# Kernel optimization log

Measured on AMD Instinct MI355X. Metric: run time of the kernel, lower is better.

The kernel has to match this reference:

```python
import jax, jax.numpy as jnp
import numpy as np

DIM = 128
NUM_HEADS = 4
WH, WW = 7, 7
N = WH * WW
B_ = 4096


def _relative_position_index():
    coords_h = np.arange(WH)
    coords_w = np.arange(WW)
    coords = np.stack(np.meshgrid(coords_h, coords_w, indexing='ij'))  # (2, Wh, Ww)
    coords_flat = coords.reshape(2, -1)  # (2, N)
    rel = coords_flat[:, :, None] - coords_flat[:, None, :]  # (2, N, N)
    rel = rel.transpose(1, 2, 0).astype(np.int32)  # (N, N, 2)
    rel[:, :, 0] += WH - 1
    rel[:, :, 1] += WW - 1
    rel[:, :, 0] *= 2 * WW - 1
    return rel.sum(-1)  # (N, N) int32


def setup_inputs() -> dict:
    key = jax.random.key(0)
    ks = jax.random.split(key, 6)
    x = jax.random.normal(ks[0], (B_, N, DIM), dtype=jnp.float32)
    # torch nn.Linear-style params: weight (out, in), bias (out,)
    qkv_w = jax.random.normal(ks[1], (3 * DIM, DIM), dtype=jnp.float32) * (DIM ** -0.5)
    qkv_b = jnp.zeros((3 * DIM,), dtype=jnp.float32)
    proj_w = jax.random.normal(ks[2], (DIM, DIM), dtype=jnp.float32) * (DIM ** -0.5)
    proj_b = jnp.zeros((DIM,), dtype=jnp.float32)
    rpb_table = jax.random.normal(ks[3], ((2 * WH - 1) * (2 * WW - 1), NUM_HEADS), dtype=jnp.float32) * 0.02
    rpi = jnp.asarray(_relative_position_index())  # (N, N) int32
    return {"x": x, "qkv_w": qkv_w, "qkv_b": qkv_b, "proj_w": proj_w,
            "proj_b": proj_b, "rpb_table": rpb_table, "rpi": rpi}


def reference(x, qkv_w, qkv_b, proj_w, proj_b, rpb_table, rpi):
    b, n, c = x.shape
    h = NUM_HEADS
    hd = c // h
    scale = hd ** -0.5
    qkv = jnp.einsum('bnc,oc->bno', x, qkv_w) + qkv_b  # (B_, N, 3C)
    qkv = qkv.reshape(b, n, 3, h, hd)
    q = jnp.transpose(qkv[:, :, 0], (0, 2, 1, 3))  # (b, h, n, hd)
    k = jnp.transpose(qkv[:, :, 1], (0, 2, 1, 3))
    v = jnp.transpose(qkv[:, :, 2], (0, 2, 1, 3))
    attn = jnp.einsum('bhnd,bhmd->bhnm', q * scale, k)  # (b, h, n, n)
    bias = rpb_table[rpi.reshape(-1)].reshape(n, n, h)  # gather bias per pair
    attn = attn + jnp.transpose(bias, (2, 0, 1))[None]  # (1, h, n, n)
    attn = jax.nn.softmax(attn, axis=-1)
    out = jnp.einsum('bhnm,bhmd->bhnd', attn, v)
    out = jnp.transpose(out, (0, 2, 1, 3)).reshape(b, n, c)
    out = jnp.einsum('bnc,oc->bno', out, proj_w) + proj_b
    return out
```

## Files before the change

### kernel.cpp

```cpp
#include <hip/hip_runtime.h>
#include <hip/hip_bf16.h>

typedef __attribute__((ext_vector_type(8))) short s16x8;
typedef __attribute__((ext_vector_type(4))) float f32x4;
typedef unsigned short u16;

#define NTOK 49
#define CDIM 128
#define NH 4
#define NWIN 4096

#define XT_STRIDE 136
#define QK_STRIDE 40
#define VT_STRIDE 72
#define HEAD_SZ 6400
#define K_OFF 2560
#define VT_OFF 4096
#define LDS_ELEMS 25600

__device__ __forceinline__ u16 f2bf(float f) {
    __hip_bfloat16 h = __float2bfloat16(f);
    return __builtin_bit_cast(u16, h);
}
__device__ __forceinline__ unsigned pk2(float a, float b) {
    return (unsigned)f2bf(a) | ((unsigned)f2bf(b) << 16);
}

__global__ void prep_kernel(const float* __restrict__ qkv_w,
                            const float* __restrict__ proj_w,
                            const float* __restrict__ rpb,
                            const int* __restrict__ rpi,
                            u16* __restrict__ pkq, u16* __restrict__ pkp,
                            float* __restrict__ bMv) {
    int idx = blockIdx.x * blockDim.x + threadIdx.x;
    if (idx < 49152) {
        int r = idx & 7, lane = (idx >> 3) & 63, tile = idx >> 9;
        int ot = tile % 24, kt = tile / 24;
        int o = ot * 16 + (lane & 15);
        int k = kt * 32 + ((lane >> 4) << 3) + r;
        pkq[idx] = f2bf(qkv_w[o * CDIM + k]);
    } else if (idx < 65536) {
        int i2 = idx - 49152;
        int r = i2 & 7, lane = (i2 >> 3) & 63, tile = i2 >> 9;
        int ot = tile & 7, kt = tile >> 3;
        int o = ot * 16 + (lane & 15);
        int k = kt * 32 + ((lane >> 4) << 3) + r;
        pkp[i2] = f2bf(proj_w[o * CDIM + k]);
    } else if (idx < 81920) {
        int i = idx - 65536;
        int r = i & 3, lr = (i >> 2) & 15, g = (i >> 6) & 3;
        int nt = (i >> 8) & 3, mt = (i >> 10) & 3, h = i >> 12;
        int q = nt * 16 + lr, j = mt * 16 + 4 * g + r;
        bMv[i] = (q < NTOK && j < NTOK) ? rpb[rpi[q * NTOK + j] * NH + h] : 0.0f;
    }
}

__global__ __launch_bounds__(256, 3) void winattn_kernel(
    const float* __restrict__ x, const float* __restrict__ qkv_b,
    const float* __restrict__ proj_b,
    const u16* __restrict__ pkq, const u16* __restrict__ pkp,
    const float* __restrict__ bMv, float* __restrict__ out) {
    __shared__ __align__(16) u16 smem[LDS_ELEMS];
    const int b = blockIdx.x;
    const int tid = threadIdx.x;
    const int wave = tid >> 6, lane = tid & 63;
    const int g = lane >> 4, lr = lane & 15;

    u16* xt = smem;

    const float* xp = x + (size_t)b * (NTOK * CDIM);
    for (int t = tid; t < (NTOK * CDIM) / 4; t += 256) {
        float4 v = reinterpret_cast<const float4*>(xp)[t];
        int lin = t * 4;
        int i = lin >> 7, c = lin & 127;
        uint2 pkv;
        pkv.x = pk2(v.x, v.y);
        pkv.y = pk2(v.z, v.w);
        *reinterpret_cast<uint2*>(&xt[i * XT_STRIDE + c]) = pkv;
    }
    for (int t = tid; t < 15 * XT_STRIDE; t += 256) xt[NTOK * XT_STRIDE + t] = 0;
    __syncthreads();

    f32x4 acc[4][6] = {};
    const s16x8* pkqv = reinterpret_cast<const s16x8*>(pkq);
#pragma unroll
    for (int kt = 0; kt < 4; ++kt) {
        s16x8 af[4];
#pragma unroll
        for (int mt = 0; mt < 4; ++mt)
            af[mt] = *reinterpret_cast<const s16x8*>(&xt[(mt * 16 + lr) * XT_STRIDE + kt * 32 + g * 8]);
        s16x8 bfr[6];
#pragma unroll
        for (int t = 0; t < 6; ++t) {
            int ot = (t >> 1) * 8 + 2 * wave + (t & 1);
            bfr[t] = pkqv[(kt * 24 + ot) * 64 + lane];
        }
#pragma unroll
        for (int mt = 0; mt < 4; ++mt)
#pragma unroll
            for (int t = 0; t < 6; ++t)
                acc[mt][t] = __builtin_amdgcn_mfma_f32_16x16x32_bf16(af[mt], bfr[t], acc[mt][t], 0, 0, 0);
    }
    __syncthreads();

    u16* hb = smem + wave * HEAD_SZ;
    u16* qb = hb;
    u16* kb = hb + K_OFF;
    const float scale = 0.17677669529663687f;
    unsigned vpk[4][2][2];
#pragma unroll
    for (int t = 0; t < 6; ++t) {
        int sel = t >> 1, t1 = t & 1;
        int o = (sel * 8 + 2 * wave + t1) * 16 + lr;
        float bias = qkv_b[o];
        int d = t1 * 16 + lr;
#pragma unroll
        for (int mt = 0; mt < 4; ++mt) {
            if (sel == 0) {
#pragma unroll
                for (int r = 0; r < 4; ++r)
                    qb[(mt * 16 + 4 * g + r) * QK_STRIDE + d] = f2bf((acc[mt][t][r] + bias) * scale);
            } else if (sel == 1) {
#pragma unroll
                for (int r = 0; r < 4; ++r)
                    kb[(mt * 16 + 4 * g + r) * QK_STRIDE + d] = f2bf(acc[mt][t][r] + bias);
            } else {
                vpk[mt][t1][0] = pk2(acc[mt][t][0] + bias, acc[mt][t][1] + bias);
                vpk[mt][t1][1] = pk2(acc[mt][t][2] + bias, acc[mt][t][3] + bias);
            }
        }
    }
    asm volatile("s_waitcnt lgkmcnt(0)" ::: "memory");

    f32x4 st[4][4] = {};
    {
        s16x8 ak[4], bq[4];
#pragma unroll
        for (int mt = 0; mt < 4; ++mt)
            ak[mt] = *reinterpret_cast<const s16x8*>(&kb[(mt * 16 + lr) * QK_STRIDE + g * 8]);
#pragma unroll
        for (int nt = 0; nt < 4; ++nt)
            bq[nt] = *reinterpret_cast<const s16x8*>(&qb[(nt * 16 + lr) * QK_STRIDE + g * 8]);
#pragma unroll
        for (int mt = 0; mt < 4; ++mt)
#pragma unroll
            for (int nt = 0; nt < 4; ++nt)
                st[mt][nt] = __builtin_amdgcn_mfma_f32_16x16x32_bf16(ak[mt], bq[nt], st[mt][nt], 0, 0, 0);
    }
    const f32x4* bv4 = reinterpret_cast<const f32x4*>(bMv);
#pragma unroll
    for (int mt = 0; mt < 4; ++mt)
#pragma unroll
        for (int nt = 0; nt < 4; ++nt) {
            f32x4 bb = bv4[(((wave * 4 + mt) * 4 + nt) * 4 + g) * 16 + lr];
#pragma unroll
            for (int r = 0; r < 4; ++r) {
                float v = st[mt][nt][r] + bb[r];
                if (mt == 3) v = (g == 0 && r == 0) ? v : -1e30f;
                st[mt][nt][r] = v;
            }
        }
#pragma unroll
    for (int nt = 0; nt < 4; ++nt) {
        float m = st[0][nt][0];
#pragma unroll
        for (int mt = 0; mt < 4; ++mt)
#pragma unroll
            for (int r = 0; r < 4; ++r) m = fmaxf(m, st[mt][nt][r]);
        m = fmaxf(m, __shfl_xor(m, 16, 64));
        m = fmaxf(m, __shfl_xor(m, 32, 64));
        float s = 0.f;
#pragma unroll
        for (int mt = 0; mt < 4; ++mt)
#pragma unroll
            for (int r = 0; r < 4; ++r) {
                float e = __expf(st[mt][nt][r] - m);
                st[mt][nt][r] = e;
                s += e;
            }
        s += __shfl_xor(s, 16, 64);
        s += __shfl_xor(s, 32, 64);
        float inv = 1.0f / s;
#pragma unroll
        for (int mt = 0; mt < 4; ++mt)
#pragma unroll
            for (int r = 0; r < 4; ++r) st[mt][nt][r] *= inv;
    }
    char* pB = reinterpret_cast<char*>(hb);
    u16* vtb = hb + VT_OFF;
#pragma unroll
    for (int mt = 0; mt < 4; ++mt)
#pragma unroll
        for (int nt = 0; nt < 4; ++nt) {
            uint2 w2;
            w2.x = pk2(st[mt][nt][0], st[mt][nt][1]);
            w2.y = pk2(st[mt][nt][2], st[mt][nt][3]);
            int q = nt * 16 + lr;
            int off = (q * 128 + mt * 32 + g * 8) ^ ((q & 7) << 4);
            *reinterpret_cast<uint2*>(pB + off) = w2;
        }
#pragma unroll
    for (int mt = 0; mt < 4; ++mt)
#pragma unroll
        for (int tv = 0; tv < 2; ++tv) {
            uint2 w2;
            w2.x = vpk[mt][tv][0];
            w2.y = vpk[mt][tv][1];
            *reinterpret_cast<uint2*>(&vtb[(tv * 16 + lr) * VT_STRIDE + mt * 16 + 4 * g]) = w2;
        }
    asm volatile("s_waitcnt lgkmcnt(0)" ::: "memory");

    f32x4 ov[4][2] = {};
    {
        s16x8 pa[4][2], bv[2][2];
#pragma unroll
        for (int qmt = 0; qmt < 4; ++qmt)
#pragma unroll
            for (int kk = 0; kk < 2; ++kk) {
                int off = (((qmt * 16 + lr) * 128) + kk * 64 + g * 16) ^ ((lr & 7) << 4);
                pa[qmt][kk] = *reinterpret_cast<const s16x8*>(pB + off);
            }
#pragma unroll
        for (int nt = 0; nt < 2; ++nt)
#pragma unroll
            for (int kk = 0; kk < 2; ++kk)
                bv[nt][kk] = *reinterpret_cast<const s16x8*>(&vtb[(nt * 16 + lr) * VT_STRIDE + kk * 32 + g * 8]);
#pragma unroll
        for (int qmt = 0; qmt < 4; ++qmt)
#pragma unroll
            for (int nt = 0; nt < 2; ++nt)
#pragma unroll
                for (int kk = 0; kk < 2; ++kk)
                    ov[qmt][nt] = __builtin_amdgcn_mfma_f32_16x16x32_bf16(pa[qmt][kk], bv[nt][kk], ov[qmt][nt], 0, 0, 0);
    }
    __syncthreads();

    u16* ao = smem;
#pragma unroll
    for (int qmt = 0; qmt < 4; ++qmt)
#pragma unroll
        for (int nt = 0; nt < 2; ++nt)
#pragma unroll
            for (int r = 0; r < 4; ++r)
                ao[(qmt * 16 + 4 * g + r) * XT_STRIDE + wave * 32 + nt * 16 + lr] = f2bf(ov[qmt][nt][r]);
    __syncthreads();

    f32x4 pacc[4][2] = {};
    const s16x8* pkpv = reinterpret_cast<const s16x8*>(pkp);
#pragma unroll
    for (int kt = 0; kt < 4; ++kt) {
        s16x8 af[4], bfr[2];
#pragma unroll
        for (int mt = 0; mt < 4; ++mt)
            af[mt] = *reinterpret_cast<const s16x8*>(&ao[(mt * 16 + lr) * XT_STRIDE + kt * 32 + g * 8]);
#pragma unroll
        for (int t = 0; t < 2; ++t)
            bfr[t] = pkpv[(kt * 8 + wave * 2 + t) * 64 + lane];
#pragma unroll
        for (int mt = 0; mt < 4; ++mt)
#pragma unroll
            for (int t = 0; t < 2; ++t)
                pacc[mt][t] = __builtin_amdgcn_mfma_f32_16x16x32_bf16(af[mt], bfr[t], pacc[mt][t], 0, 0, 0);
    }
    float* outp = out + (size_t)b * (NTOK * CDIM);
#pragma unroll
    for (int t = 0; t < 2; ++t) {
        int oc = (wave * 2 + t) * 16 + lr;
        float pbv = proj_b[oc];
#pragma unroll
        for (int mt = 0; mt < 4; ++mt)
#pragma unroll
            for (int r = 0; r < 4; ++r) {
                int i = mt * 16 + 4 * g + r;
                if (i < NTOK) outp[(size_t)i * CDIM + oc] = pacc[mt][t][r] + pbv;
            }
    }
}

extern "C" void kernel_launch(void* const* d_in, const int* in_sizes, int n_in,
                              void* d_out, int out_size, void* d_ws, size_t ws_size,
                              hipStream_t stream) {
    const float* x      = (const float*)d_in[0];
    const float* qkv_w  = (const float*)d_in[1];
    const float* qkv_b  = (const float*)d_in[2];
    const float* proj_w = (const float*)d_in[3];
    const float* proj_b = (const float*)d_in[4];
    const float* rpb    = (const float*)d_in[5];
    const int*   rpi    = (const int*)d_in[6];
    float* out = (float*)d_out;

    u16*   pkq = (u16*)d_ws;
    u16*   pkp = pkq + 49152;
    float* bMv = (float*)((char*)d_ws + 131072);

    prep_kernel<<<320, 256, 0, stream>>>(qkv_w, proj_w, rpb, rpi, pkq, pkp, bMv);
    winattn_kernel<<<NWIN, 256, 0, stream>>>(x, qkv_b, proj_b, pkq, pkp, bMv, out);
}
```

Baseline: 102.2 us.

## Load x directly into MFMA fragments, use exp2 softmax, transpose PV, add setprio

Drops the LDS staging of x and builds the bf16 A-fragments straight from global float4 loads, which removes a block-wide barrier and an LDS round trip. The softmax now uses exp2 with log2e folded into the scale and the bias table. The PV matmul is transposed so the attention output can be written to LDS as packed 8-byte stores, and the proj weight fragments are prefetched before the barrier. s_setprio is wrapped around the MFMA bursts. The risk is that direct global loads are less coalesced and raise register pressure under the 3-block occupancy target.

```diff
diff --git a/kernel.cpp b/kernel.cpp
--- a/kernel.cpp
+++ b/kernel.cpp
@@ -9,8 +9,9 @@
 #define CDIM 128
 #define NH 4
 #define NWIN 4096
-
-#define XT_STRIDE 136
+#define LOG2E 1.4426950408889634f
+
+#define AO_STRIDE 136
 #define QK_STRIDE 40
 #define VT_STRIDE 72
 #define HEAD_SZ 6400
@@ -51,7 +52,7 @@
         int r = i & 3, lr = (i >> 2) & 15, g = (i >> 6) & 3;
         int nt = (i >> 8) & 3, mt = (i >> 10) & 3, h = i >> 12;
         int q = nt * 16 + lr, j = mt * 16 + 4 * g + r;
-        bMv[i] = (q < NTOK && j < NTOK) ? rpb[rpi[q * NTOK + j] * NH + h] : 0.0f;
+        bMv[i] = (q < NTOK && j < NTOK) ? rpb[rpi[q * NTOK + j] * NH + h] * LOG2E : 0.0f;
     }
 }
 
@@ -65,21 +66,7 @@
     const int tid = threadIdx.x;
     const int wave = tid >> 6, lane = tid & 63;
     const int g = lane >> 4, lr = lane & 15;
-
-    u16* xt = smem;
-
     const float* xp = x + (size_t)b * (NTOK * CDIM);
-    for (int t = tid; t < (NTOK * CDIM) / 4; t += 256) {
-        float4 v = reinterpret_cast<const float4*>(xp)[t];
-        int lin = t * 4;
-        int i = lin >> 7, c = lin & 127;
-        uint2 pkv;
-        pkv.x = pk2(v.x, v.y);
-        pkv.y = pk2(v.z, v.w);
-        *reinterpret_cast<uint2*>(&xt[i * XT_STRIDE + c]) = pkv;
-    }
-    for (int t = tid; t < 15 * XT_STRIDE; t += 256) xt[NTOK * XT_STRIDE + t] = 0;
-    __syncthreads();
 
     f32x4 acc[4][6] = {};
     const s16x8* pkqv = reinterpret_cast<const s16x8*>(pkq);
@@ -87,26 +74,39 @@
     for (int kt = 0; kt < 4; ++kt) {
         s16x8 af[4];
 #pragma unroll
-        for (int mt = 0; mt < 4; ++mt)
-            af[mt] = *reinterpret_cast<const s16x8*>(&xt[(mt * 16 + lr) * XT_STRIDE + kt * 32 + g * 8]);
+        for (int mt = 0; mt < 4; ++mt) {
+            int row = mt * 16 + lr;
+            if (row < NTOK) {
+                const float* p = xp + row * CDIM + kt * 32 + g * 8;
+                float4 a0 = *reinterpret_cast<const float4*>(p);
+                float4 a1 = *reinterpret_cast<const float4*>(p + 4);
+                union { s16x8 v; unsigned u[4]; } t;
+                t.u[0] = pk2(a0.x, a0.y); t.u[1] = pk2(a0.z, a0.w);
+                t.u[2] = pk2(a1.x, a1.y); t.u[3] = pk2(a1.z, a1.w);
+                af[mt] = t.v;
+            } else {
+                af[mt] = (s16x8)(short)0;
+            }
+        }
         s16x8 bfr[6];
 #pragma unroll
         for (int t = 0; t < 6; ++t) {
             int ot = (t >> 1) * 8 + 2 * wave + (t & 1);
             bfr[t] = pkqv[(kt * 24 + ot) * 64 + lane];
         }
+        __builtin_amdgcn_s_setprio(1);
 #pragma unroll
         for (int mt = 0; mt < 4; ++mt)
 #pragma unroll
             for (int t = 0; t < 6; ++t)
                 acc[mt][t] = __builtin_amdgcn_mfma_f32_16x16x32_bf16(af[mt], bfr[t], acc[mt][t], 0, 0, 0);
-    }
-    __syncthreads();
+        __builtin_amdgcn_s_setprio(0);
+    }
 
     u16* hb = smem + wave * HEAD_SZ;
     u16* qb = hb;
     u16* kb = hb + K_OFF;
-    const float scale = 0.17677669529663687f;
+    const float scale = 0.17677669529663687f * LOG2E;
     unsigned vpk[4][2][2];
 #pragma unroll
     for (int t = 0; t < 6; ++t) {
@@ -141,11 +141,13 @@
 #pragma unroll
         for (int nt = 0; nt < 4; ++nt)
             bq[nt] = *reinterpret_cast<const s16x8*>(&qb[(nt * 16 + lr) * QK_STRIDE + g * 8]);
+        __builtin_amdgcn_s_setprio(1);
 #pragma unroll
         for (int mt = 0; mt < 4; ++mt)
 #pragma unroll
             for (int nt = 0; nt < 4; ++nt)
                 st[mt][nt] = __builtin_amdgcn_mfma_f32_16x16x32_bf16(ak[mt], bq[nt], st[mt][nt], 0, 0, 0);
+        __builtin_amdgcn_s_setprio(0);
     }
     const f32x4* bv4 = reinterpret_cast<const f32x4*>(bMv);
 #pragma unroll
@@ -174,7 +176,7 @@
         for (int mt = 0; mt < 4; ++mt)
 #pragma unroll
             for (int r = 0; r < 4; ++r) {
-                float e = __expf(st[mt][nt][r] - m);
+                float e = exp2f(st[mt][nt][r] - m);
                 st[mt][nt][r] = e;
                 s += e;
             }
@@ -210,57 +212,68 @@
         }
     asm volatile("s_waitcnt lgkmcnt(0)" ::: "memory");
 
-    f32x4 ov[4][2] = {};
+    f32x4 ov[2][4] = {};
     {
-        s16x8 pa[4][2], bv[2][2];
-#pragma unroll
-        for (int qmt = 0; qmt < 4; ++qmt)
+        s16x8 va[2][2], pbf[4][2];
+#pragma unroll
+        for (int mtd = 0; mtd < 2; ++mtd)
+#pragma unroll
+            for (int kk = 0; kk < 2; ++kk)
+                va[mtd][kk] = *reinterpret_cast<const s16x8*>(&vtb[(mtd * 16 + lr) * VT_STRIDE + kk * 32 + g * 8]);
+#pragma unroll
+        for (int nt = 0; nt < 4; ++nt)
 #pragma unroll
             for (int kk = 0; kk < 2; ++kk) {
-                int off = (((qmt * 16 + lr) * 128) + kk * 64 + g * 16) ^ ((lr & 7) << 4);
-                pa[qmt][kk] = *reinterpret_cast<const s16x8*>(pB + off);
-            }
-#pragma unroll
-        for (int nt = 0; nt < 2; ++nt)
-#pragma unroll
-            for (int kk = 0; kk < 2; ++kk)
-                bv[nt][kk] = *reinterpret_cast<const s16x8*>(&vtb[(nt * 16 + lr) * VT_STRIDE + kk * 32 + g * 8]);
-#pragma unroll
-        for (int qmt = 0; qmt < 4; ++qmt)
-#pragma unroll
-            for (int nt = 0; nt < 2; ++nt)
+                int off = (((nt * 16 + lr) * 128) + kk * 64 + g * 16) ^ ((lr & 7) << 4);
+                pbf[nt][kk] = *reinterpret_cast<const s16x8*>(pB + off);
+            }
+        __builtin_amdgcn_s_setprio(1);
+#pragma unroll
+        for (int mtd = 0; mtd < 2; ++mtd)
+#pragma unroll
+            for (int nt = 0; nt < 4; ++nt)
 #pragma unroll
                 for (int kk = 0; kk < 2; ++kk)
-                    ov[qmt][nt] = __builtin_amdgcn_mfma_f32_16x16x32_bf16(pa[qmt][kk], bv[nt][kk], ov[qmt][nt], 0, 0, 0);
-    }
+                    ov[mtd][nt] = __builtin_amdgcn_mfma_f32_16x16x32_bf16(va[mtd][kk], pbf[nt][kk], ov[mtd][nt], 0, 0, 0);
+        __builtin_amdgcn_s_setprio(0);
+    }
+
+    s16x8 pfr[4][2];
+    const s16x8* pkpv = reinterpret_cast<const s16x8*>(pkp);
+#pragma unroll
+    for (int kt = 0; kt < 4; ++kt)
+#pragma unroll
+        for (int t = 0; t < 2; ++t)
+            pfr[kt][t] = pkpv[(kt * 8 + wave * 2 + t) * 64 + lane];
+
     __syncthreads();
 
     u16* ao = smem;
 #pragma unroll
-    for (int qmt = 0; qmt < 4; ++qmt)
-#pragma unroll
-        for (int nt = 0; nt < 2; ++nt)
-#pragma unroll
-            for (int r = 0; r < 4; ++r)
-                ao[(qmt * 16 + 4 * g + r) * XT_STRIDE + wave * 32 + nt * 16 + lr] = f2bf(ov[qmt][nt][r]);
+    for (int mtd = 0; mtd < 2; ++mtd)
+#pragma unroll
+        for (int nt = 0; nt < 4; ++nt) {
+            uint2 w2;
+            w2.x = pk2(ov[mtd][nt][0], ov[mtd][nt][1]);
+            w2.y = pk2(ov[mtd][nt][2], ov[mtd][nt][3]);
+            *reinterpret_cast<uint2*>(&ao[(nt * 16 + lr) * AO_STRIDE + wave * 32 + mtd * 16 + 4 * g]) = w2;
+        }
     __syncthreads();
 
     f32x4 pacc[4][2] = {};
-    const s16x8* pkpv = reinterpret_cast<const s16x8*>(pkp);
 #pragma unroll
     for (int kt = 0; kt < 4; ++kt) {
-        s16x8 af[4], bfr[2];
-#pragma unroll
-        for (int mt = 0; mt < 4; ++mt)
-            af[mt] = *reinterpret_cast<const s16x8*>(&ao[(mt * 16 + lr) * XT_STRIDE + kt * 32 + g * 8]);
-#pragma unroll
-        for (int t = 0; t < 2; ++t)
-            bfr[t] = pkpv[(kt * 8 + wave * 2 + t) * 64 + lane];
+        s16x8 af[4];
+#pragma unroll
+        for (int mt = 0; mt < 4; ++mt)
+            af[mt] = *reinterpret_cast<const s16x8*>(&ao[(mt * 16 + lr) * AO_STRIDE + kt * 32 + g * 8]);
+        __builtin_amdgcn_s_setprio(1);
 #pragma unroll
         for (int mt = 0; mt < 4; ++mt)
 #pragma unroll
             for (int t = 0; t < 2; ++t)
-                pacc[mt][t] = __builtin_amdgcn_mfma_f32_16x16x32_bf16(af[mt], bfr[t], pacc[mt][t], 0, 0, 0);
+                pacc[mt][t] = __builtin_amdgcn_mfma_f32_16x16x32_bf16(af[mt], pfr[kt][t], pacc[mt][t], 0, 0, 0);
+        __builtin_amdgcn_s_setprio(0);
     }
     float* outp = out + (size_t)b * (NTOK * CDIM);
 #pragma unroll
```

After: 142.9 us. 39.9% more time.
